# Optimization experiments

Measured on AMD Instinct MI355X. Metric: run time of the kernel, lower is better.

## Reference

```python
import jax, jax.numpy as jnp
import numpy as np


def setup_inputs() -> dict:
    key = jax.random.key(0)
    ks = jax.random.split(key, 5)
    B, NINS, NHID = 128, 4096, 128
    inputs = jax.random.normal(ks[0], (B, NINS, NHID), dtype=jnp.float32)
    claims = jax.random.normal(ks[1], (B, NHID), dtype=jnp.float32)  # unused by forward
    # project: Linear(2*nhid -> 64) -> ReLU -> Linear(64 -> 1)
    W1 = jax.random.normal(ks[2], (2 * NHID, 64), dtype=jnp.float32) * (1.0 / np.sqrt(2 * NHID))
    b1 = jnp.zeros((64,), dtype=jnp.float32)
    W2 = jax.random.normal(ks[3], (64, 1), dtype=jnp.float32) * (1.0 / np.sqrt(64))
    b2 = jnp.zeros((1,), dtype=jnp.float32)
    return {"inputs": inputs, "index": 5, "claims": claims,
            "W1": W1, "b1": b1, "W2": W2, "b2": b2}


def reference(inputs, index, claims, W1, b1, W2, b2):
    # inputs: [B, nins, nhid]
    B, NINS, NHID = inputs.shape
    own = jax.lax.dynamic_slice_in_dim(inputs, index, 1, axis=1)  # [B, 1, nhid]
    own = jnp.broadcast_to(own, (B, NINS, NHID))                  # repeat over nins
    tmp = jnp.concatenate([own, inputs], axis=2)                  # [B, nins, 2*nhid]
    h = jax.nn.relu(jnp.einsum('bnd,dk->bnk', tmp, W1) + b1)      # [B, nins, 64]
    att = jnp.einsum('bnk,ko->bno', h, W2) + b2                   # [B, nins, 1]
    weights = jax.nn.softmax(att[..., 0], axis=1)                 # [B, nins]
    outputs = jnp.einsum('bnd,bn->bd', inputs, weights)           # [B, nhid]
    return outputs
```

## Files before the change

### kernel.cpp

```cpp
#include <hip/hip_runtime.h>
#include <math.h>

#define BATCH 128
#define NINS  4096
#define NHID  128
#define KH    64
#define NPART 128
#define PART_STRIDE 136
#define O_OFF 8
#define TPW 2
#define XP 136

typedef __attribute__((ext_vector_type(8))) short short8;
typedef __attribute__((ext_vector_type(4))) float f32x4;
typedef __attribute__((ext_vector_type(4))) unsigned int u32x4;

__device__ inline unsigned short f2bf(float f) {
    union { float f; unsigned u; } v; v.f = f;
    return (unsigned short)((v.u + 0x7FFFu + ((v.u >> 16) & 1u)) >> 16);
}

__device__ inline unsigned cvt_pk_u32(float a, float b) {
#if __has_builtin(__builtin_amdgcn_cvt_pk_bf16_f32)
    typedef __attribute__((ext_vector_type(2))) __bf16 bf16x2;
    bf16x2 p = __builtin_amdgcn_cvt_pk_bf16_f32(a, b);
    unsigned u; __builtin_memcpy(&u, &p, 4); return u;
#else
    return (unsigned)f2bf(a) | ((unsigned)f2bf(b) << 16);
#endif
}

__global__ void precompute_c(const float* __restrict__ inputs,
                             const int* __restrict__ index_p,
                             const float* __restrict__ W1,
                             const float* __restrict__ b1,
                             float* __restrict__ c) {
    const int b = blockIdx.x;
    const int k = threadIdx.x;
    const int idx = index_p[0];
    const float* own = inputs + ((size_t)b * NINS + idx) * NHID;
    float acc = b1[k];
    #pragma unroll 8
    for (int d = 0; d < NHID; ++d)
        acc = fmaf(own[d], W1[d * KH + k], acc);
    c[b * KH + k] = acc;
}

__global__ __launch_bounds__(256, 4)
void att_partial(const float* __restrict__ inputs,
                 const float* __restrict__ W1,
                 const float* __restrict__ W2,
                 const float* __restrict__ b2_p,
                 const float* __restrict__ c,
                 float* __restrict__ part) {
    __shared__ unsigned short WbT[KH][XP];
    __shared__ float ebuf[4][32];

    const int tid  = threadIdx.x;
    const int lane = tid & 63;
    const int wv   = tid >> 6;
    const int b    = blockIdx.y;
    const int quad = lane >> 4;
    const int m16  = lane & 15;

    const float* xb = inputs + (size_t)b * NINS * NHID;

    {
        const int n  = tid >> 2;
        const int kb = (tid & 3) * 32;
        const float* wp = W1 + (size_t)(NHID + kb) * KH + n;
        #pragma unroll
        for (int j = 0; j < 32; j += 2) {
            unsigned u = cvt_pk_u32(wp[(size_t)j * KH], wp[(size_t)(j + 1) * KH]);
            *(unsigned*)&WbT[n][kb + j] = u;
        }
    }
    __syncthreads();

    float w2v[4];
    #pragma unroll
    for (int nf = 0; nf < 4; ++nf) w2v[nf] = W2[nf * 16 + m16];
    const float b2v = b2_p[0];
    float cv[4];
    #pragma unroll
    for (int nf = 0; nf < 4; ++nf) cv[nf] = c[b * KH + nf * 16 + m16];

    const int base = (blockIdx.x * 4 + wv) * TPW;

    f32x4 raw[2][4][2];
    short8 Af[2][4];

    auto load_raw = [&](int n0) {
        #pragma unroll
        for (int mf = 0; mf < 2; ++mf) {
            const float* rp = xb + (size_t)(n0 + mf * 16 + m16) * NHID + quad * 8;
            #pragma unroll
            for (int ks = 0; ks < 4; ++ks) {
                raw[mf][ks][0] = *(const f32x4*)(rp + ks * 32);
                raw[mf][ks][1] = *(const f32x4*)(rp + ks * 32 + 4);
            }
        }
    };
    auto cvt_raw = [&]() {
        #pragma unroll
        for (int mf = 0; mf < 2; ++mf)
            #pragma unroll
            for (int ks = 0; ks < 4; ++ks) {
                u32x4 u;
                u.x = cvt_pk_u32(raw[mf][ks][0].x, raw[mf][ks][0].y);
                u.y = cvt_pk_u32(raw[mf][ks][0].z, raw[mf][ks][0].w);
                u.z = cvt_pk_u32(raw[mf][ks][1].x, raw[mf][ks][1].y);
                u.w = cvt_pk_u32(raw[mf][ks][1].z, raw[mf][ks][1].w);
                __builtin_memcpy(&Af[mf][ks], &u, 16);
            }
    };

    load_raw(base * 32);
    cvt_raw();

    #pragma unroll
    for (int t = 0; t < TPW; ++t) {
        const int tile = base + t;
        const int n0   = tile * 32;

        f32x4 acc[2][4];
        #pragma unroll
        for (int mf = 0; mf < 2; ++mf)
            #pragma unroll
            for (int nf = 0; nf < 4; ++nf) {
                f32x4 z = {cv[nf], cv[nf], cv[nf], cv[nf]};
                acc[mf][nf] = z;
            }

        #pragma unroll
        for (int ks = 0; ks < 4; ++ks) {
            short8 Bf[4];
            #pragma unroll
            for (int nf = 0; nf < 4; ++nf)
                Bf[nf] = *(const short8*)&WbT[nf * 16 + m16][ks * 32 + quad * 8];
            #pragma unroll
            for (int mf = 0; mf < 2; ++mf)
                #pragma unroll
                for (int nf = 0; nf < 4; ++nf)
                    acc[mf][nf] = __builtin_amdgcn_mfma_f32_16x16x32_bf16(
                        Af[mf][ks], Bf[nf], acc[mf][nf], 0, 0, 0);
        }

        float att[2][4];
        #pragma unroll
        for (int mf = 0; mf < 2; ++mf)
            #pragma unroll
            for (int r = 0; r < 4; ++r) {
                float s = 0.0f;
                #pragma unroll
                for (int nf = 0; nf < 4; ++nf)
                    s = fmaf(fmaxf(acc[mf][nf][r], 0.0f), w2v[nf], s);
                s += __shfl_xor(s, 1);
                s += __shfl_xor(s, 2);
                s += __shfl_xor(s, 4);
                s += __shfl_xor(s, 8);
                att[mf][r] = s + b2v;
            }

        if (t + 1 < TPW) load_raw((tile + 1) * 32);

        float ev[2][4];
        float L = 0.0f;
        #pragma unroll
        for (int mf = 0; mf < 2; ++mf)
            #pragma unroll
            for (int r = 0; r < 4; ++r) {
                ev[mf][r] = __expf(att[mf][r]);
                L += ev[mf][r];
            }
        L += __shfl_xor(L, 16);
        L += __shfl_xor(L, 32);

        if (m16 == 0) {
            #pragma unroll
            for (int mf = 0; mf < 2; ++mf)
                #pragma unroll
                for (int r = 0; r < 4; ++r)
                    ebuf[wv][mf * 16 + quad * 4 + r] = ev[mf][r];
        }

        if (t + 1 < TPW) cvt_raw();

        const int G  = lane >> 5;
        const int db = (lane & 31) * 4;
        f32x4 e4[4];
        #pragma unroll
        for (int i = 0; i < 4; ++i)
            e4[i] = *(const f32x4*)&ebuf[wv][G * 16 + i * 4];

        f32x4 o = {0.0f, 0.0f, 0.0f, 0.0f};
        const float* xr = xb + (size_t)(n0 + G * 16) * NHID + db;
        #pragma unroll
        for (int jj = 0; jj < 16; ++jj) {
            f32x4 xv = *(const f32x4*)(xr + (size_t)jj * NHID);
            o += xv * e4[jj >> 2][jj & 3];
        }
        #pragma unroll
        for (int i = 0; i < 4; ++i) o[i] += __shfl_xor(o[i], 32);

        float* p = part + (size_t)(b * NPART + tile) * PART_STRIDE;
        if (lane == 0) p[0] = L;
        if (lane < 32) *(f32x4*)(p + O_OFF + db) = o;
    }
}

__global__ void finalize(const float* __restrict__ part,
                         float* __restrict__ out) {
    __shared__ float wred[2];

    const int b = blockIdx.x;
    const int d = threadIdx.x;
    const float* pb = part + (size_t)b * NPART * PART_STRIDE;

    float s = pb[(size_t)d * PART_STRIDE];
    s += __shfl_xor(s, 1);
    s += __shfl_xor(s, 2);
    s += __shfl_xor(s, 4);
    s += __shfl_xor(s, 8);
    s += __shfl_xor(s, 16);
    s += __shfl_xor(s, 32);
    if ((d & 63) == 0) wred[d >> 6] = s;
    __syncthreads();
    const float S = wred[0] + wred[1];

    float acc = 0.0f;
    #pragma unroll 8
    for (int p = 0; p < NPART; ++p)
        acc += pb[(size_t)p * PART_STRIDE + O_OFF + d];
    out[b * NHID + d] = acc / S;
}

extern "C" void kernel_launch(void* const* d_in, const int* in_sizes, int n_in,
                              void* d_out, int out_size, void* d_ws, size_t ws_size,
                              hipStream_t stream) {
    const float* inputs = (const float*)d_in[0];
    const int*   index  = (const int*)  d_in[1];
    const float* W1     = (const float*)d_in[3];
    const float* b1     = (const float*)d_in[4];
    const float* W2     = (const float*)d_in[5];
    const float* b2     = (const float*)d_in[6];
    float* out = (float*)d_out;

    float* c    = (float*)d_ws;
    float* part = c + BATCH * KH;

    precompute_c<<<dim3(BATCH), dim3(64), 0, stream>>>(inputs, index, W1, b1, c);

    dim3 gB(NPART / (4 * TPW), BATCH);
    att_partial<<<gB, dim3(256), 0, stream>>>(inputs, W1, W2, b2, c, part);

    finalize<<<dim3(BATCH), dim3(NHID), 0, stream>>>(part, out);
}
```

Baseline: 406.8 us.

## Fuse own-row projection into attention kernel and drop manual prefetch

```diff
diff --git a/kernel.cpp b/kernel.cpp
--- a/kernel.cpp
+++ b/kernel.cpp
@@ -30,30 +30,16 @@
 #endif
 }
 
-__global__ void precompute_c(const float* __restrict__ inputs,
-                             const int* __restrict__ index_p,
-                             const float* __restrict__ W1,
-                             const float* __restrict__ b1,
-                             float* __restrict__ c) {
-    const int b = blockIdx.x;
-    const int k = threadIdx.x;
-    const int idx = index_p[0];
-    const float* own = inputs + ((size_t)b * NINS + idx) * NHID;
-    float acc = b1[k];
-    #pragma unroll 8
-    for (int d = 0; d < NHID; ++d)
-        acc = fmaf(own[d], W1[d * KH + k], acc);
-    c[b * KH + k] = acc;
-}
-
 __global__ __launch_bounds__(256, 4)
 void att_partial(const float* __restrict__ inputs,
+                 const int* __restrict__ index_p,
                  const float* __restrict__ W1,
+                 const float* __restrict__ b1,
                  const float* __restrict__ W2,
                  const float* __restrict__ b2_p,
-                 const float* __restrict__ c,
                  float* __restrict__ part) {
     __shared__ unsigned short WbT[KH][XP];
+    __shared__ float csp[4][KH];
     __shared__ float ebuf[4][32];
 
     const int tid  = threadIdx.x;
@@ -75,6 +61,18 @@
             *(unsigned*)&WbT[n][kb + j] = u;
         }
     }
+
+    {
+        const int kk = lane;
+        const int dq = wv;
+        const int idx = index_p[0];
+        const float* own = xb + (size_t)idx * NHID;
+        float ca = (dq == 0) ? b1[kk] : 0.0f;
+        #pragma unroll 8
+        for (int d = dq * 32; d < dq * 32 + 32; ++d)
+            ca = fmaf(own[d], W1[(size_t)d * KH + kk], ca);
+        csp[dq][kk] = ca;
+    }
     __syncthreads();
 
     float w2v[4];
@@ -83,45 +81,34 @@
     const float b2v = b2_p[0];
     float cv[4];
     #pragma unroll
-    for (int nf = 0; nf < 4; ++nf) cv[nf] = c[b * KH + nf * 16 + m16];
+    for (int nf = 0; nf < 4; ++nf) {
+        const int kk = nf * 16 + m16;
+        cv[nf] = (csp[0][kk] + csp[1][kk]) + (csp[2][kk] + csp[3][kk]);
+    }
 
     const int base = (blockIdx.x * 4 + wv) * TPW;
-
-    f32x4 raw[2][4][2];
-    short8 Af[2][4];
-
-    auto load_raw = [&](int n0) {
-        #pragma unroll
-        for (int mf = 0; mf < 2; ++mf) {
-            const float* rp = xb + (size_t)(n0 + mf * 16 + m16) * NHID + quad * 8;
-            #pragma unroll
-            for (int ks = 0; ks < 4; ++ks) {
-                raw[mf][ks][0] = *(const f32x4*)(rp + ks * 32);
-                raw[mf][ks][1] = *(const f32x4*)(rp + ks * 32 + 4);
-            }
-        }
-    };
-    auto cvt_raw = [&]() {
-        #pragma unroll
-        for (int mf = 0; mf < 2; ++mf)
-            #pragma unroll
-            for (int ks = 0; ks < 4; ++ks) {
-                u32x4 u;
-                u.x = cvt_pk_u32(raw[mf][ks][0].x, raw[mf][ks][0].y);
-                u.y = cvt_pk_u32(raw[mf][ks][0].z, raw[mf][ks][0].w);
-                u.z = cvt_pk_u32(raw[mf][ks][1].x, raw[mf][ks][1].y);
-                u.w = cvt_pk_u32(raw[mf][ks][1].z, raw[mf][ks][1].w);
-                __builtin_memcpy(&Af[mf][ks], &u, 16);
-            }
-    };
-
-    load_raw(base * 32);
-    cvt_raw();
 
     #pragma unroll
     for (int t = 0; t < TPW; ++t) {
         const int tile = base + t;
         const int n0   = tile * 32;
+
+        short8 Af[2][4];
+        #pragma unroll
+        for (int mf = 0; mf < 2; ++mf) {
+            const float* rp = xb + (size_t)(n0 + mf * 16 + m16) * NHID + quad * 8;
+            #pragma unroll
+            for (int ks = 0; ks < 4; ++ks) {
+                f32x4 v0 = *(const f32x4*)(rp + ks * 32);
+                f32x4 v1 = *(const f32x4*)(rp + ks * 32 + 4);
+                u32x4 u;
+                u.x = cvt_pk_u32(v0.x, v0.y);
+                u.y = cvt_pk_u32(v0.z, v0.w);
+                u.z = cvt_pk_u32(v1.x, v1.y);
+                u.w = cvt_pk_u32(v1.z, v1.w);
+                __builtin_memcpy(&Af[mf][ks], &u, 16);
+            }
+        }
 
         f32x4 acc[2][4];
         #pragma unroll
@@ -162,8 +149,6 @@
                 att[mf][r] = s + b2v;
             }
 
-        if (t + 1 < TPW) load_raw((tile + 1) * 32);
-
         float ev[2][4];
         float L = 0.0f;
         #pragma unroll
@@ -183,8 +168,6 @@
                 for (int r = 0; r < 4; ++r)
                     ebuf[wv][mf * 16 + quad * 4 + r] = ev[mf][r];
         }
-
-        if (t + 1 < TPW) cvt_raw();
 
         const int G  = lane >> 5;
         const int db = (lane & 31) * 4;
@@ -246,13 +229,10 @@
     const float* b2     = (const float*)d_in[6];
     float* out = (float*)d_out;
 
-    float* c    = (float*)d_ws;
-    float* part = c + BATCH * KH;
-
-    precompute_c<<<dim3(BATCH), dim3(64), 0, stream>>>(inputs, index, W1, b1, c);
+    float* part = (float*)d_ws;
 
     dim3 gB(NPART / (4 * TPW), BATCH);
-    att_partial<<<gB, dim3(256), 0, stream>>>(inputs, W1, W2, b2, c, part);
+    att_partial<<<gB, dim3(256), 0, stream>>>(inputs, index, W1, b1, W2, b2, part);
 
     finalize<<<dim3(BATCH), dim3(NHID), 0, stream>>>(part, out);
 }
```

After: 386.8 us. -4.9%, faster.
